# Optimization experiments

Measured on AMD Instinct MI355X. Metric: run time of the kernel, lower is better.

Reference implementation:

```python
import jax, jax.numpy as jnp
import numpy as np
import math

N, D, F, G = 8192, 512, 2048, 102
GAMMA = 0.5
NEG = -1e9


def setup_inputs() -> dict:
    key = jax.random.key(0)
    ks = jax.random.split(key, 32)
    x = jax.random.normal(ks[0], (N, D), dtype=jnp.float32)
    real_edge_mask = jax.random.bernoulli(ks[1], 0.9, (N, N))  # True = masked (non-edge)
    fake_edge_mask = jax.random.bernoulli(ks[2], 0.1, (N, N))
    # per-row distinct sorted drop indices over gene_list = arange(D)
    r = jax.random.uniform(ks[3], (N, D))
    drop_idx = jnp.sort(jnp.argsort(r, axis=1)[:, :G], axis=1).astype(jnp.int32)
    s = 1.0 / math.sqrt(D)
    def W(k, m, n):
        return jax.random.normal(k, (m, n), dtype=jnp.float32) * s
    inp = {
        'x': x, 'drop_idx': drop_idx,
        'real_edge_mask': real_edge_mask, 'fake_edge_mask': fake_edge_mask,
        'enc_Wq_r': W(ks[4], D, D), 'enc_Wk_r': W(ks[5], D, D),
        'enc_Wq_f': W(ks[6], D, D), 'enc_Wk_f': W(ks[7], D, D), 'enc_Wv': W(ks[8], D, D),
        'dec_Wq_r': W(ks[9], D, D), 'dec_Wk_r': W(ks[10], D, D),
        'dec_Wq_f': W(ks[11], D, D), 'dec_Wk_f': W(ks[12], D, D), 'dec_Wv': W(ks[13], D, D),
        'ff_W1': W(ks[14], D, F), 'ff_b1': jnp.zeros((F,), jnp.float32),
        'ff_W2': W(ks[15], F, D), 'ff_b2': jnp.zeros((D,), jnp.float32),
        'ln1_g': jnp.ones((D,), jnp.float32), 'ln1_b': jnp.zeros((D,), jnp.float32),
        'ln2_g': jnp.ones((D,), jnp.float32), 'ln2_b': jnp.zeros((D,), jnp.float32),
        'ln3_g': jnp.ones((D,), jnp.float32), 'ln3_b': jnp.zeros((D,), jnp.float32),
        'head_W': W(ks[16], D, D), 'head_b': jnp.zeros((D,), jnp.float32),
    }
    return inp


def layer_norm(h, g, b, eps=1e-5):
    mu = h.mean(-1, keepdims=True)
    var = ((h - mu) ** 2).mean(-1, keepdims=True)
    return (h - mu) * jax.lax.rsqrt(var + eps) * g + b


def spatial_attention(h, Wq_r, Wk_r, Wq_f, Wk_f, Wv, rmask, fmask, gamma):
    d = h.shape[-1]
    scale = 1.0 / math.sqrt(d)
    sr = jnp.where(rmask, NEG, (h @ Wq_r) @ (h @ Wk_r).T * scale)  # [N,N]
    sf = jnp.where(fmask, NEG, (h @ Wq_f) @ (h @ Wk_f).T * scale)  # [N,N]
    m = jnp.maximum(sr.max(axis=1, keepdims=True), sf.max(axis=1, keepdims=True))
    scores = (jnp.exp(sr - m) + gamma * jnp.exp(sf - m)) / (1.0 + gamma)
    attn = scores / scores.sum(axis=-1, keepdims=True)
    return attn @ (h @ Wv), attn


def reference(x, drop_idx, real_edge_mask, fake_edge_mask,
              enc_Wq_r, enc_Wk_r, enc_Wq_f, enc_Wk_f, enc_Wv,
              dec_Wq_r, dec_Wk_r, dec_Wq_f, dec_Wk_f, dec_Wv,
              ff_W1, ff_b1, ff_W2, ff_b2,
              ln1_g, ln1_b, ln2_g, ln2_b, ln3_g, ln3_b,
              head_W, head_b):
    rows = jnp.arange(x.shape[0])[:, None]
    drop_x = x.at[rows, drop_idx].set(0.0)
    hidden, _ = spatial_attention(drop_x, enc_Wq_r, enc_Wk_r, enc_Wq_f, enc_Wk_f, enc_Wv,
                                  real_edge_mask, fake_edge_mask, GAMMA)
    hidden = layer_norm(hidden + drop_x, ln1_g, ln1_b)
    ff = jax.nn.gelu(hidden @ ff_W1 + ff_b1, approximate=False) @ ff_W2 + ff_b2
    hidden = layer_norm(hidden + ff, ln2_g, ln2_b)
    recon, _ = spatial_attention(hidden, dec_Wq_r, dec_Wk_r, dec_Wq_f, dec_Wk_f, dec_Wv,
                                 real_edge_mask, fake_edge_mask, GAMMA)
    recon = layer_norm(recon + hidden, ln3_g, ln3_b)
    h = recon @ head_W + head_b
    x_init = jnp.take_along_axis(x, drop_idx, axis=1)    # [N,G]
    x_recon = jnp.take_along_axis(h, drop_idx, axis=1)   # [N,G]
    return x_init, x_recon
```

## Files before the change

### kernel.cpp

```cpp
#include <hip/hip_runtime.h>
#include <cstdint>
#include <cstddef>


typedef unsigned short u16;
typedef __bf16 bf16x8 __attribute__((ext_vector_type(8)));
typedef float f32x4 __attribute__((ext_vector_type(4)));

#define GAMMA_C 0.5f
#define SCALE_C 0.04419417382415922f
#define NG      (8192 * 102)
#define SLAB    ((size_t)8192 * 512)

__device__ __forceinline__ float b2f(u16 u) {
  union { unsigned int i; float f; } c; c.i = ((unsigned int)u) << 16; return c.f;
}
__device__ __forceinline__ u16 f2b(float f) {
  union { float f; unsigned int i; } c; c.f = f;
  unsigned int u = c.i + 0x7FFFu + ((c.i >> 16) & 1u);
  return (u16)(u >> 16);
}
__device__ __forceinline__ float gelu_exact(float x) {
  return 0.5f * x * (1.0f + erff(x * 0.70710678118654752f));
}
__device__ __forceinline__ int idx_at(const void* p, int i, int i64) {
  return i64 ? (int)((const long long*)p)[i] : ((const int*)p)[i];
}
__device__ __forceinline__ float fl_at(const void* p, size_t i, int f32m) {
  return f32m ? ((const float*)p)[i] : b2f(((const u16*)p)[i]);
}
__device__ __forceinline__ void mask8(const void* m, size_t base, int f, bool o[8]) {
  if (f == 1) {
    unsigned long long v = *(const unsigned long long*)((const unsigned char*)m + base);
#pragma unroll
    for (int e = 0; e < 8; ++e) o[e] = ((v >> (8 * e)) & 0xFF) != 0;
  } else if (f == 0) {
    const uint4 a = *(const uint4*)((const int*)m + base);
    const uint4 b = *(const uint4*)((const int*)m + base + 4);
    o[0] = a.x; o[1] = a.y; o[2] = a.z; o[3] = a.w;
    o[4] = b.x; o[5] = b.y; o[6] = b.z; o[7] = b.w;
  } else if (f == 2) {
    const uint4 v = *(const uint4*)((const u16*)m + base);
    const u16* p = (const u16*)&v;
#pragma unroll
    for (int e = 0; e < 8; ++e) o[e] = p[e] != 0;
  } else {
    const uint4 a = *(const uint4*)((const float*)m + base);
    const uint4 b = *(const uint4*)((const float*)m + base + 4);
    o[0] = a.x; o[1] = a.y; o[2] = a.z; o[3] = a.w;
    o[4] = b.x; o[5] = b.y; o[6] = b.z; o[7] = b.w;
  }
}

#define GLD16(g, l) __builtin_amdgcn_global_load_lds(                         \
    (const __attribute__((address_space(1))) void*)(g),                       \
    (__attribute__((address_space(3))) void*)(l), 16, 0, 0)

__global__ void detect_all(const unsigned char* __restrict__ rmask,
                           const void* __restrict__ xin,
                           const void* __restrict__ idx,
                           int* __restrict__ flags) {
  __shared__ int nz[4];
  __shared__ int mx, bl;
  const int t = threadIdx.x;
  if (t < 4) nz[t] = 0;
  if (t == 0) { mx = 0; bl = 0; }
  __syncthreads();
  int cnt = 0, lm = 0;
  for (int i = t; i < 4096; i += 256) {
    const int v = rmask[i];
    if (v) { ++cnt; if (v > lm) lm = v; }
  }
  if (cnt) atomicAdd(&nz[t & 3], cnt);
  if (lm) atomicMax(&mx, lm);
  int bcnt = 0;
  for (int i = t; i < 2048; i += 256) {
    const u16 u = ((const u16*)xin)[2 * i];
    const int e = (u >> 7) & 0xFF;
    if ((e >= 110 && e <= 141) || u == 0) ++bcnt;
  }
  atomicAdd(&bl, bcnt);
  __syncthreads();
  if (t == 0) {
    int f;
    if (nz[1] == 0 && nz[2] == 0 && nz[3] == 0) f = 0;
    else if (nz[0] == 0 && nz[1] == 0) f = 3;
    else if (mx <= 1) f = 1;
    else f = 2;
    flags[0] = f;
    flags[2] = (bl >= 1536) ? 0 : 1;
    int ok = 1, prev = -1;
    for (int j = 0; j < 102; ++j) {
      const int v = ((const int*)idx)[j];
      if (v <= prev || v < 0 || v >= 512) { ok = 0; break; }
      prev = v;
    }
    flags[1] = ok ? 0 : 1;
  }
}

__global__ void bitmask_prep(const void* __restrict__ mr, const void* __restrict__ mf,
                             unsigned char* __restrict__ bmr, unsigned char* __restrict__ bmf,
                             const int* __restrict__ flags) {
  const int i = blockIdx.x * 256 + threadIdx.x;
  const int f = flags[0];
  bool mk[8];
  mask8(mr, (size_t)i * 8, f, mk);
  unsigned char b = 0;
#pragma unroll
  for (int e = 0; e < 8; ++e) b |= (unsigned char)mk[e] << e;
  bmr[i] = b;
  mask8(mf, (size_t)i * 8, f, mk);
  b = 0;
#pragma unroll
  for (int e = 0; e < 8; ++e) b |= (unsigned char)mk[e] << e;
  bmf[i] = b;
}

struct PtrPack { const void* p[11]; };
__global__ void transpose_cvt_b(PtrPack srcs, u16* __restrict__ out,
                                const int* __restrict__ flags) {
  __shared__ u16 tile[32][33];
  const void* in = srcs.p[blockIdx.z];
  u16* o = out + (size_t)blockIdx.z * 512 * 512;
  const int f32m = flags[2];
  const int c0 = blockIdx.x * 32, r0 = blockIdx.y * 32;
  const int tx = threadIdx.x, ty = threadIdx.y;
  for (int i = ty; i < 32; i += 8) {
    const size_t src = (size_t)(r0 + i) * 512 + (c0 + tx);
    tile[i][tx] = f32m ? f2b(((const float*)in)[src]) : ((const u16*)in)[src];
  }
  __syncthreads();
  for (int i = ty; i < 32; i += 8)
    o[(size_t)(c0 + i) * 512 + (r0 + tx)] = tile[tx][i];
}
__global__ void transpose_cvt(const void* __restrict__ in, u16* __restrict__ out,
                              int R, int C, const int* __restrict__ flags) {
  __shared__ u16 tile[32][33];
  const int f32m = flags[2];
  const int c0 = blockIdx.x * 32, r0 = blockIdx.y * 32;
  const int tx = threadIdx.x, ty = threadIdx.y;
  for (int i = ty; i < 32; i += 8) {
    const size_t src = (size_t)(r0 + i) * C + (c0 + tx);
    tile[i][tx] = f32m ? f2b(((const float*)in)[src]) : ((const u16*)in)[src];
  }
  __syncthreads();
  for (int i = ty; i < 32; i += 8)
    out[(size_t)(c0 + i) * R + (r0 + tx)] = tile[tx][i];
}

__global__ void cvt_to_bf16(const void* __restrict__ in, u16* __restrict__ out,
                            int n, const int* __restrict__ flags) {
  const int i = blockIdx.x * blockDim.x + threadIdx.x;
  if (i < n)
    out[i] = flags[2] ? f2b(((const float*)in)[i]) : ((const u16*)in)[i];
}
__global__ void zero_f32(float* __restrict__ p, int n) {
  const int i = blockIdx.x * blockDim.x + threadIdx.x;
  if (i < n) p[i] = 0.f;
}
__global__ void zero_drop(u16* __restrict__ dx, const void* __restrict__ idx,
                          const int* __restrict__ flags) {
  const int i = blockIdx.x * blockDim.x + threadIdx.x;
  if (i < NG) {
    const int row = i / 102;
    dx[(size_t)row * 512 + idx_at(idx, i, flags[1])] = 0;
  }
}
__global__ void gather_out_k(const void* __restrict__ x, const u16* __restrict__ hs,
                             const void* __restrict__ hb,
                             const void* __restrict__ idx, void* __restrict__ out,
                             const int* __restrict__ flags) {
  const int i = blockIdx.x * blockDim.x + threadIdx.x;
  if (i < NG) {
    const int row = i / 102;
    const int c = idx_at(idx, i, flags[1]);
    const size_t src = (size_t)row * 512 + c;
    const float hv = b2f(hs[src]) + b2f(hs[src + SLAB]) + fl_at(hb, c, flags[2]);
    if (flags[2]) {
      ((float*)out)[i] = ((const float*)x)[src];
      ((float*)out)[NG + i] = hv;
    } else {
      ((u16*)out)[i] = ((const u16*)x)[src];
      ((u16*)out)[NG + i] = f2b(hv);
    }
  }
}

__global__ __launch_bounds__(256, 4)
void gemm_bt(const u16* __restrict__ A, int lda,
             const u16* __restrict__ Bt, int ldb,
             u16* __restrict__ C, int ldc,
             int K, int mode, const void* __restrict__ bias,
             const int* __restrict__ flags, u16* __restrict__ aux,
             long long slabStride) {
  __shared__ alignas(16) u16 smem[16384];
  u16* As = smem;
  u16* Bs = smem + 8192;
  const int tid = threadIdx.x;
  const int lane = tid & 63, wave = tid >> 6;
  const int l15 = lane & 15, l4 = lane >> 4;
  const int wm = (wave >> 1) << 6, wn = (wave & 1) << 6;
  const int m0 = blockIdx.y << 7, n0 = blockIdx.x << 7;
  const size_t kShift = (size_t)blockIdx.z * (size_t)K;
  C += (size_t)blockIdx.z * (size_t)slabStride;

  f32x4 acc[4][4];
#pragma unroll
  for (int i = 0; i < 4; ++i)
#pragma unroll
    for (int j = 0; j < 4; ++j) acc[i][j] = (f32x4){0.f, 0.f, 0.f, 0.f};

  const int lrow = lane >> 3;
  const int lcg = (lane & 7) ^ lrow;
  const u16* aG = A + kShift + (size_t)(m0 + wave * 8 + lrow) * lda + lcg * 8;
  const u16* bG = Bt + kShift + (size_t)(n0 + wave * 8 + lrow) * ldb + lcg * 8;
  u16* asDst = &As[(wave * 8) * 64];
  u16* bsDst = &Bs[(wave * 8) * 64];
  const int swz = (l15 & 7) << 3;

  for (int k0 = 0; k0 < K; k0 += 64) {
#pragma unroll
    for (int r = 0; r < 4; ++r) {
      GLD16(aG + (size_t)(r * 32) * lda + k0, asDst + r * 32 * 64);
      GLD16(bG + (size_t)(r * 32) * ldb + k0, bsDst + r * 32 * 64);
    }
    __syncthreads();
#pragma unroll
    for (int kk = 0; kk < 2; ++kk) {
      bf16x8 a[4], b[4];
      const int koff = (((kk << 2) + l4) << 3) ^ swz;
#pragma unroll
      for (int i = 0; i < 4; ++i) {
        a[i] = *(const bf16x8*)&As[(wm + (i << 4) + l15) * 64 + koff];
        b[i] = *(const bf16x8*)&Bs[(wn + (i << 4) + l15) * 64 + koff];
      }
#pragma unroll
      for (int i = 0; i < 4; ++i)
#pragma unroll
        for (int j = 0; j < 4; ++j)
          acc[i][j] = __builtin_amdgcn_mfma_f32_16x16x32_bf16(a[i], b[j], acc[i][j], 0, 0, 0);
    }
    __syncthreads();
  }

  const int f32m = flags[2];

  if (mode == 2 && n0 >= 2048) {
#pragma unroll
    for (int i = 0; i < 4; ++i) {
      const int rbase = m0 + wm + (i << 4) + l4 * 4;
#pragma unroll
      for (int j = 0; j < 4; ++j) {
        const int gn = n0 - 2048 + wn + (j << 4) + l15;
        ushort4 pk;
        pk.x = f2b(acc[i][j][0]); pk.y = f2b(acc[i][j][1]);
        pk.z = f2b(acc[i][j][2]); pk.w = f2b(acc[i][j][3]);
        *(ushort4*)&aux[(size_t)gn * 8192 + rbase] = pk;
      }
    }
    return;
  }

#pragma unroll
  for (int i = 0; i < 4; ++i) {
    const int rl0 = wm + (i << 4) + l4 * 4;
#pragma unroll
    for (int j = 0; j < 4; ++j) {
      const int cl = wn + (j << 4) + l15;
      float bv = 0.f;
      if (bias) bv = fl_at(bias, n0 + cl, f32m);
      const int chunk = cl >> 3, within = cl & 7;
#pragma unroll
      for (int r = 0; r < 4; ++r) {
        const int rl = rl0 + r;
        float v = acc[i][j][r] + bv;
        if (mode == 1) v = gelu_exact(v);
        const int wchunk = (chunk & 8) | ((chunk ^ rl) & 7);
        smem[rl * 128 + wchunk * 8 + within] = f2b(v);
      }
    }
  }
  __syncthreads();

  const int r = tid >> 1, h = tid & 1;
  const int grow = m0 + r;
#pragma unroll
  for (int cb = 0; cb < 8; ++cb) {
    const int chunkidx = h * 8 + cb;
    const int rchunk = (chunkidx & 8) | ((chunkidx ^ r) & 7);
    uint4 raw = *(const uint4*)&smem[r * 128 + rchunk * 8];
    *(uint4*)&C[(size_t)grow * ldc + n0 + chunkidx * 8] = raw;
  }
}

__global__ __launch_bounds__(256, 4)
void score_fused(const u16* __restrict__ P,
                 const unsigned char* __restrict__ bmr,
                 const unsigned char* __restrict__ bmf,
                 u16* __restrict__ W, float* __restrict__ lvec) {
  __shared__ alignas(16) u16 stage[16384];
  __shared__ unsigned long long mrs[256], mfs[256];
  const int tid = threadIdx.x;
  const int lane = tid & 63, wave = tid >> 6;
  const int l15 = lane & 15, l4 = lane >> 4;
  const int wm = (wave >> 1) << 6, wn = (wave & 1) << 6;
  const int m0 = blockIdx.y << 7, n0 = blockIdx.x << 7;

  {
    const int r = tid >> 1, hh = tid & 1;
    const size_t mo = (size_t)(m0 + r) * 1024 + (n0 >> 3) + hh * 8;
    mrs[tid] = *(const unsigned long long*)&bmr[mo];
    mfs[tid] = *(const unsigned long long*)&bmf[mo];
  }

  const int lrow = lane >> 3;
  const int lcg = (lane & 7) ^ lrow;
  const int swz = (l15 & 7) << 3;
  u16* asDst = &stage[(wave * 8) * 64];
  u16* bsDst = &stage[8192 + (wave * 8) * 64];

  unsigned int srp[4][4][2];
  f32x4 acc[4][4];

  for (int p = 0; p < 2; ++p) {
#pragma unroll
    for (int i = 0; i < 4; ++i)
#pragma unroll
      for (int j = 0; j < 4; ++j) acc[i][j] = (f32x4){0.f, 0.f, 0.f, 0.f};

    const u16* aG = P + (p ? 1024 : 0) + (size_t)(m0 + wave * 8 + lrow) * 2048 + lcg * 8;
    const u16* bG = P + (p ? 1536 : 512) + (size_t)(n0 + wave * 8 + lrow) * 2048 + lcg * 8;

    for (int k0 = 0; k0 < 512; k0 += 64) {
#pragma unroll
      for (int r = 0; r < 4; ++r) {
        GLD16(aG + (size_t)(r * 32) * 2048 + k0, asDst + r * 32 * 64);
        GLD16(bG + (size_t)(r * 32) * 2048 + k0, bsDst + r * 32 * 64);
      }
      __syncthreads();
#pragma unroll
      for (int kk = 0; kk < 2; ++kk) {
        bf16x8 a[4], b[4];
        const int koff = (((kk << 2) + l4) << 3) ^ swz;
#pragma unroll
        for (int i = 0; i < 4; ++i) {
          a[i] = *(const bf16x8*)&stage[(wm + (i << 4) + l15) * 64 + koff];
          b[i] = *(const bf16x8*)&stage[8192 + (wn + (i << 4) + l15) * 64 + koff];
        }
#pragma unroll
        for (int i = 0; i < 4; ++i)
#pragma unroll
          for (int j = 0; j < 4; ++j)
            acc[i][j] = __builtin_amdgcn_mfma_f32_16x16x32_bf16(a[i], b[j], acc[i][j], 0, 0, 0);
      }
      __syncthreads();
    }

    if (p == 0) {
#pragma unroll
      for (int i = 0; i < 4; ++i)
#pragma unroll
        for (int j = 0; j < 4; ++j) {
          srp[i][j][0] = (unsigned int)f2b(acc[i][j][0] * SCALE_C)
                       | ((unsigned int)f2b(acc[i][j][1] * SCALE_C) << 16);
          srp[i][j][1] = (unsigned int)f2b(acc[i][j][2] * SCALE_C)
                       | ((unsigned int)f2b(acc[i][j][3] * SCALE_C) << 16);
        }
    }
  }

  const int hb = wn >> 6;
#pragma unroll
  for (int i = 0; i < 4; ++i) {
    const int rl0 = wm + (i << 4) + l4 * 4;
#pragma unroll
    for (int r = 0; r < 4; ++r) {
      const int rl = rl0 + r;
      const unsigned long long mr = mrs[rl * 2 + hb];
      const unsigned long long mf = mfs[rl * 2 + hb];
      float rsum = 0.f;
#pragma unroll
      for (int j = 0; j < 4; ++j) {
        const int cl = wn + (j << 4) + l15;
        const int bit = cl & 63;
        const float srv = b2f((u16)(srp[i][j][r >> 1] >> ((r & 1) * 16)));
        const float sfv = acc[i][j][r] * SCALE_C;
        const float wr = ((mr >> bit) & 1) ? 0.f : __expf(srv);
        const float wf = ((mf >> bit) & 1) ? 0.f : __expf(sfv);
        const float w = wr + GAMMA_C * wf;
        rsum += w;
        const int chunk = cl >> 3, within = cl & 7;
        const int wchunk = (chunk & 8) | ((chunk ^ rl) & 7);
        stage[rl * 128 + wchunk * 8 + within] = f2b(w);
      }
      rsum += __shfl_xor(rsum, 1);
      rsum += __shfl_xor(rsum, 2);
      rsum += __shfl_xor(rsum, 4);
      rsum += __shfl_xor(rsum, 8);
      if (l15 == 0) atomicAdd(&lvec[m0 + rl], rsum);
    }
  }
  __syncthreads();

  const int rr = tid >> 1, hh = tid & 1;
  const int grow = m0 + rr;
#pragma unroll
  for (int cb = 0; cb < 8; ++cb) {
    const int chunkidx = hh * 8 + cb;
    const int rchunk = (chunkidx & 8) | ((chunkidx ^ rr) & 7);
    uint4 raw = *(const uint4*)&stage[rr * 128 + rchunk * 8];
    *(uint4*)&W[(size_t)grow * 8192 + n0 + chunkidx * 8] = raw;
  }
}

__global__ __launch_bounds__(256)
void pv_ln(const u16* __restrict__ slabs, const float* __restrict__ lvec,
           const u16* __restrict__ res, const void* __restrict__ g,
           const void* __restrict__ be, u16* __restrict__ out,
           const int* __restrict__ flags) {
  const int row = blockIdx.x, tid = threadIdx.x;
  const int f32m = flags[2];
  const size_t off = (size_t)row * 512 + tid * 2;
  const float linv = 1.0f / lvec[row];
  float o0 = 0.f, o1 = 0.f;
#pragma unroll
  for (int s = 0; s < 8; ++s) {
    o0 += b2f(slabs[off + s * SLAB]);
    o1 += b2f(slabs[off + 1 + s * SLAB]);
  }
  const float v0 = o0 * linv + b2f(res[off]);
  const float v1 = o1 * linv + b2f(res[off + 1]);
  __shared__ float r1[256], r2[256];
  r1[tid] = v0 + v1;
  r2[tid] = v0 * v0 + v1 * v1;
  __syncthreads();
  for (int s = 128; s > 0; s >>= 1) {
    if (tid < s) { r1[tid] += r1[tid + s]; r2[tid] += r2[tid + s]; }
    __syncthreads();
  }
  const float mu = r1[0] * (1.f / 512.f);
  const float var = r2[0] * (1.f / 512.f) - mu * mu;
  const float rs = rsqrtf(var + 1e-5f);
  out[off]     = f2b((v0 - mu) * rs * fl_at(g, tid * 2, f32m)     + fl_at(be, tid * 2, f32m));
  out[off + 1] = f2b((v1 - mu) * rs * fl_at(g, tid * 2 + 1, f32m) + fl_at(be, tid * 2 + 1, f32m));
}

__global__ __launch_bounds__(256)
void ff_ln(const u16* __restrict__ slabs, const void* __restrict__ bias,
           const u16* __restrict__ res, const void* __restrict__ g,
           const void* __restrict__ be, u16* __restrict__ out,
           const int* __restrict__ flags) {
  const int row = blockIdx.x, tid = threadIdx.x;
  const int f32m = flags[2];
  const size_t off = (size_t)row * 512 + tid * 2;
  const float v0 = b2f(slabs[off]) + b2f(slabs[off + SLAB])
                 + fl_at(bias, tid * 2, f32m) + b2f(res[off]);
  const float v1 = b2f(slabs[off + 1]) + b2f(slabs[off + 1 + SLAB])
                 + fl_at(bias, tid * 2 + 1, f32m) + b2f(res[off + 1]);
  __shared__ float r1[256], r2[256];
  r1[tid] = v0 + v1;
  r2[tid] = v0 * v0 + v1 * v1;
  __syncthreads();
  for (int s = 128; s > 0; s >>= 1) {
    if (tid < s) { r1[tid] += r1[tid + s]; r2[tid] += r2[tid + s]; }
    __syncthreads();
  }
  const float mu = r1[0] * (1.f / 512.f);
  const float var = r2[0] * (1.f / 512.f) - mu * mu;
  const float rs = rsqrtf(var + 1e-5f);
  out[off]     = f2b((v0 - mu) * rs * fl_at(g, tid * 2, f32m)     + fl_at(be, tid * 2, f32m));
  out[off + 1] = f2b((v1 - mu) * rs * fl_at(g, tid * 2 + 1, f32m) + fl_at(be, tid * 2 + 1, f32m));
}

extern "C" void kernel_launch(void* const* d_in, const int* in_sizes, int n_in,
                              void* d_out, int out_size, void* d_ws, size_t ws_size,
                              hipStream_t stream) {
  (void)in_sizes; (void)n_in; (void)out_size; (void)ws_size;
  const void* x = d_in[0];
  const void* dropidx = d_in[1];
  const void* rmask = d_in[2];
  const void* fmask = d_in[3];

  char* base = (char*)d_ws;
  size_t cur = 0;
  auto alloc = [&](size_t b) -> void* {
    void* p = base + cur;
    cur += (b + 255) & ~(size_t)255;
    return p;
  };

  int* flags = (int*)alloc(256);
  u16* Wt = (u16*)alloc((size_t)11 * 512 * 512 * 2);
  u16* wff1t = (u16*)alloc((size_t)2048 * 512 * 2);
  u16* wff2t = (u16*)alloc((size_t)512 * 2048 * 2);
  const size_t ND2 = (size_t)8192 * 512 * 2;
  u16* dropx = (u16*)alloc(ND2);
  u16* P = (u16*)alloc((size_t)8192 * 2048 * 2);
  u16* Vt = (u16*)alloc(ND2);
  u16* H1 = (u16*)alloc(ND2);
  u16* H2 = (u16*)alloc(ND2);
  u16* FF1 = (u16*)alloc((size_t)8192 * 2048 * 2);
  unsigned char* bmr = (unsigned char*)alloc((size_t)8192 * 1024);
  unsigned char* bmf = (unsigned char*)alloc((size_t)8192 * 1024);
  float* lvec = (float*)alloc((size_t)8192 * 4);
  u16* slabs = (u16*)alloc((size_t)8 * SLAB * 2);
  u16* Wb = (u16*)alloc((size_t)8192 * 8192 * 2);

  detect_all<<<1, 256, 0, stream>>>((const unsigned char*)rmask, x, dropidx, flags);
  bitmask_prep<<<32768, 256, 0, stream>>>(rmask, fmask, bmr, bmf, flags);

  const dim3 tb(32, 8);
  PtrPack wp;
  for (int i = 0; i < 5; ++i) wp.p[i] = d_in[4 + i];
  for (int i = 0; i < 5; ++i) wp.p[5 + i] = d_in[9 + i];
  wp.p[10] = d_in[24];
  transpose_cvt_b<<<dim3(16, 16, 11), tb, 0, stream>>>(wp, Wt, flags);
  transpose_cvt<<<dim3(64, 16), tb, 0, stream>>>(d_in[14], wff1t, 512, 2048, flags);
  transpose_cvt<<<dim3(16, 64), tb, 0, stream>>>(d_in[16], wff2t, 2048, 512, flags);

  cvt_to_bf16<<<(8192 * 512 + 255) / 256, 256, 0, stream>>>(x, dropx, 8192 * 512, flags);
  zero_drop<<<(NG + 255) / 256, 256, 0, stream>>>(dropx, dropidx, flags);

  auto gemm = [&](const u16* A, int lda, const u16* Bt, int ldb, u16* Cc, int ldc,
                  int M, int Nn, int K, int mode, const void* bias, u16* aux,
                  int zc, long long slabStride) {
    gemm_bt<<<dim3(Nn / 128, M / 128, zc), 256, 0, stream>>>(
        A, lda, Bt, ldb, Cc, ldc, K, mode, bias, flags, aux, slabStride);
  };

  auto attention = [&](const u16* Hin, const u16* Wqkv, const void* lnG,
                       const void* lnB, u16* outLN) {
    zero_f32<<<32, 256, 0, stream>>>(lvec, 8192);
    gemm(Hin, 512, Wqkv, 512, P, 2048, 8192, 2560, 512, 2, nullptr, Vt, 1, 0);
    score_fused<<<dim3(64, 64), 256, 0, stream>>>(P, bmr, bmf, Wb, lvec);
    gemm(Wb, 8192, Vt, 8192, slabs, 512, 8192, 512, 1024, 0, nullptr, nullptr,
         8, (long long)SLAB);
    pv_ln<<<8192, 256, 0, stream>>>(slabs, lvec, Hin, lnG, lnB, outLN, flags);
  };

  attention(dropx, Wt, d_in[18], d_in[19], H1);
  gemm(H1, 512, wff1t, 512, FF1, 2048, 8192, 2048, 512, 1, d_in[15], nullptr, 1, 0);
  gemm(FF1, 2048, wff2t, 2048, slabs, 512, 8192, 512, 1024, 0, nullptr, nullptr,
       2, (long long)SLAB);
  ff_ln<<<8192, 256, 0, stream>>>(slabs, d_in[17], H1, d_in[20], d_in[21], H2, flags);
  attention(H2, Wt + (size_t)5 * 512 * 512, d_in[22], d_in[23], H1);
  gemm(H1, 512, Wt + (size_t)10 * 512 * 512, 512, slabs, 512, 8192, 512, 256, 0,
       nullptr, nullptr, 2, (long long)SLAB);
  gather_out_k<<<(NG + 255) / 256, 256, 0, stream>>>(x, slabs, d_in[25], dropidx,
                                                     d_out, flags);
}
```

Measured before the change: 1.602 ms.

## Add dedicated 128x256 split-K PV GEMM with row-interleaved slabs and 4-row LayerNorm

Replaces the generic gemm_bt call for the attention P·V product with pv_big, a 512-thread kernel using a 128x256 tile and a direct async global-to-LDS load. It writes each split-K slab in a 4-row-interleaved layout so the new pv_ln4 kernel can read four rows per thread with one vector load, and it reduces with wave shuffles instead of a shared-memory tree. The wider N tile is meant to reuse the A (score) tile across more output columns and cut redundant reads of the large score matrix. Launch bounds are also relaxed for gemm_bt and score_fused, which lets the compiler use more registers at the cost of lower occupancy.

```diff
diff --git a/kernel.cpp b/kernel.cpp
--- a/kernel.cpp
+++ b/kernel.cpp
@@ -187,7 +187,7 @@
   }
 }
 
-__global__ __launch_bounds__(256, 4)
+__global__ __launch_bounds__(256)
 void gemm_bt(const u16* __restrict__ A, int lda,
              const u16* __restrict__ Bt, int ldb,
              u16* __restrict__ C, int ldc,
@@ -294,7 +294,7 @@
   }
 }
 
-__global__ __launch_bounds__(256, 4)
+__global__ __launch_bounds__(256, 3)
 void score_fused(const u16* __restrict__ P,
                  const unsigned char* __restrict__ bmr,
                  const unsigned char* __restrict__ bmf,
@@ -414,36 +414,120 @@
   }
 }
 
-__global__ __launch_bounds__(256)
-void pv_ln(const u16* __restrict__ slabs, const float* __restrict__ lvec,
-           const u16* __restrict__ res, const void* __restrict__ g,
-           const void* __restrict__ be, u16* __restrict__ out,
-           const int* __restrict__ flags) {
-  const int row = blockIdx.x, tid = threadIdx.x;
+__global__ __launch_bounds__(512)
+void pv_big(const u16* __restrict__ W, const u16* __restrict__ Vt,
+            u16* __restrict__ slabs) {
+  __shared__ alignas(16) u16 smem[24576];
+  u16* As = smem;
+  u16* Bs = smem + 8192;
+  const int tid = threadIdx.x;
+  const int lane = tid & 63, wave = tid >> 6;
+  const int l15 = lane & 15, l4 = lane >> 4;
+  const int wm = (wave >> 2) << 6;
+  const int wn = (wave & 3) << 6;
+  const int m0 = blockIdx.y << 7, n0 = blockIdx.x << 8;
+  const int kbase = blockIdx.z << 10;
+  u16* slab = slabs + (size_t)blockIdx.z * SLAB;
+
+  f32x4 acc[4][4];
+#pragma unroll
+  for (int i = 0; i < 4; ++i)
+#pragma unroll
+    for (int j = 0; j < 4; ++j) acc[i][j] = (f32x4){0.f, 0.f, 0.f, 0.f};
+
+  const int lrow = lane >> 3;
+  const int lcg = (lane & 7) ^ lrow;
+  const u16* aG = W + (size_t)(m0 + wave * 8 + lrow) * 8192 + kbase + lcg * 8;
+  const u16* bG = Vt + (size_t)(n0 + wave * 8 + lrow) * 8192 + kbase + lcg * 8;
+  u16* asDst = &As[(wave * 8) * 64];
+  u16* bsDst = &Bs[(wave * 8) * 64];
+  const int swz = (l15 & 7) << 3;
+
+  for (int k0 = 0; k0 < 1024; k0 += 64) {
+#pragma unroll
+    for (int r = 0; r < 2; ++r)
+      GLD16(aG + (size_t)(r * 64) * 8192 + k0, asDst + r * 64 * 64);
+#pragma unroll
+    for (int r = 0; r < 4; ++r)
+      GLD16(bG + (size_t)(r * 64) * 8192 + k0, bsDst + r * 64 * 64);
+    __syncthreads();
+#pragma unroll
+    for (int kk = 0; kk < 2; ++kk) {
+      bf16x8 a[4], b[4];
+      const int koff = (((kk << 2) + l4) << 3) ^ swz;
+#pragma unroll
+      for (int i = 0; i < 4; ++i) {
+        a[i] = *(const bf16x8*)&As[(wm + (i << 4) + l15) * 64 + koff];
+        b[i] = *(const bf16x8*)&Bs[(wn + (i << 4) + l15) * 64 + koff];
+      }
+#pragma unroll
+      for (int i = 0; i < 4; ++i)
+#pragma unroll
+        for (int j = 0; j < 4; ++j)
+          acc[i][j] = __builtin_amdgcn_mfma_f32_16x16x32_bf16(a[i], b[j], acc[i][j], 0, 0, 0);
+    }
+    __syncthreads();
+  }
+
+#pragma unroll
+  for (int i = 0; i < 4; ++i) {
+    const int rbase = m0 + wm + (i << 4) + l4 * 4;
+#pragma unroll
+    for (int j = 0; j < 4; ++j) {
+      const int gn = n0 + wn + (j << 4) + l15;
+      ushort4 pk;
+      pk.x = f2b(acc[i][j][0]); pk.y = f2b(acc[i][j][1]);
+      pk.z = f2b(acc[i][j][2]); pk.w = f2b(acc[i][j][3]);
+      *(ushort4*)&slab[((size_t)(rbase >> 2) * 512 + gn) * 4] = pk;
+    }
+  }
+}
+
+__global__ __launch_bounds__(512)
+void pv_ln4(const u16* __restrict__ slabs, const float* __restrict__ lvec,
+            const u16* __restrict__ res, const void* __restrict__ g,
+            const void* __restrict__ be, u16* __restrict__ out,
+            const int* __restrict__ flags) {
+  const int gid = blockIdx.x;
+  const int col = threadIdx.x;
+  const int lane = col & 63, wave = col >> 6;
   const int f32m = flags[2];
-  const size_t off = (size_t)row * 512 + tid * 2;
-  const float linv = 1.0f / lvec[row];
-  float o0 = 0.f, o1 = 0.f;
+  float o[4] = {0.f, 0.f, 0.f, 0.f};
+  const size_t base = ((size_t)gid * 512 + col) * 4;
 #pragma unroll
   for (int s = 0; s < 8; ++s) {
-    o0 += b2f(slabs[off + s * SLAB]);
-    o1 += b2f(slabs[off + 1 + s * SLAB]);
-  }
-  const float v0 = o0 * linv + b2f(res[off]);
-  const float v1 = o1 * linv + b2f(res[off + 1]);
-  __shared__ float r1[256], r2[256];
-  r1[tid] = v0 + v1;
-  r2[tid] = v0 * v0 + v1 * v1;
-  __syncthreads();
-  for (int s = 128; s > 0; s >>= 1) {
-    if (tid < s) { r1[tid] += r1[tid + s]; r2[tid] += r2[tid + s]; }
-    __syncthreads();
-  }
-  const float mu = r1[0] * (1.f / 512.f);
-  const float var = r2[0] * (1.f / 512.f) - mu * mu;
-  const float rs = rsqrtf(var + 1e-5f);
-  out[off]     = f2b((v0 - mu) * rs * fl_at(g, tid * 2, f32m)     + fl_at(be, tid * 2, f32m));
-  out[off + 1] = f2b((v1 - mu) * rs * fl_at(g, tid * 2 + 1, f32m) + fl_at(be, tid * 2 + 1, f32m));
+    const ushort4 v = *(const ushort4*)&slabs[s * SLAB + base];
+    o[0] += b2f(v.x); o[1] += b2f(v.y); o[2] += b2f(v.z); o[3] += b2f(v.w);
+  }
+  float v[4];
+#pragma unroll
+  for (int q = 0; q < 4; ++q) {
+    const int grow = gid * 4 + q;
+    v[q] = o[q] / lvec[grow] + b2f(res[(size_t)grow * 512 + col]);
+  }
+  __shared__ float s1[4][8], s2[4][8];
+#pragma unroll
+  for (int q = 0; q < 4; ++q) {
+    float sm = v[q], sq = v[q] * v[q];
+#pragma unroll
+    for (int d = 1; d < 64; d <<= 1) {
+      sm += __shfl_xor(sm, d);
+      sq += __shfl_xor(sq, d);
+    }
+    if (lane == 0) { s1[q][wave] = sm; s2[q][wave] = sq; }
+  }
+  __syncthreads();
+  const float gv = fl_at(g, col, f32m), bv = fl_at(be, col, f32m);
+#pragma unroll
+  for (int q = 0; q < 4; ++q) {
+    float sm = 0.f, sq = 0.f;
+#pragma unroll
+    for (int w = 0; w < 8; ++w) { sm += s1[q][w]; sq += s2[q][w]; }
+    const float mu = sm * (1.f / 512.f);
+    const float var = sq * (1.f / 512.f) - mu * mu;
+    const float rs = rsqrtf(var + 1e-5f);
+    out[(size_t)(gid * 4 + q) * 512 + col] = f2b((v[q] - mu) * rs * gv + bv);
+  }
 }
 
 __global__ __launch_bounds__(256)
@@ -534,9 +618,8 @@
     zero_f32<<<32, 256, 0, stream>>>(lvec, 8192);
     gemm(Hin, 512, Wqkv, 512, P, 2048, 8192, 2560, 512, 2, nullptr, Vt, 1, 0);
     score_fused<<<dim3(64, 64), 256, 0, stream>>>(P, bmr, bmf, Wb, lvec);
-    gemm(Wb, 8192, Vt, 8192, slabs, 512, 8192, 512, 1024, 0, nullptr, nullptr,
-         8, (long long)SLAB);
-    pv_ln<<<8192, 256, 0, stream>>>(slabs, lvec, Hin, lnG, lnB, outLN, flags);
+    pv_big<<<dim3(2, 64, 8), 512, 0, stream>>>(Wb, Vt, slabs);
+    pv_ln4<<<2048, 512, 0, stream>>>(slabs, lvec, Hin, lnG, lnB, outLN, flags);
   };
 
   attention(dropx, Wt, d_in[18], d_in[19], H1);
```

Result: faster. 1.446 ms (-9.7%).
